# Kernel optimization log

Hardware: AMD Instinct MI355X
Metric: run time of the kernel (lower is better)

The kernel has to match this reference:

```python
import jax, jax.numpy as jnp
import numpy as np

NQ = 4
DIM = 1 << NQ  # 16 statevector amplitudes

def _cnot_perm(c, t):
    idx = np.arange(DIM)
    cbit = (idx >> (NQ - 1 - c)) & 1
    return np.where(cbit == 1, idx ^ (1 << (NQ - 1 - t)), idx)

# BasicEntanglerLayers CNOT ring: (0,1),(1,2),(2,3),(3,0)
CNOT_PERMS = [jnp.asarray(_cnot_perm(q, (q + 1) % NQ)) for q in range(NQ)]
_idx = np.arange(DIM)
SIGNS = jnp.asarray(np.stack([1.0 - 2.0 * ((_idx >> (NQ - 1 - q)) & 1) for q in range(NQ)]).astype(np.float32))  # (NQ, DIM), PauliZ eigenvalues


def _apply_rx(state, theta, q):
    """Apply RX(theta) on wire q. state: (N, DIM) complex64. theta: scalar or (N,)."""
    half = theta * 0.5
    c = jnp.cos(half).astype(jnp.complex64)
    js = (1j * jnp.sin(half)).astype(jnp.complex64)
    if jnp.ndim(theta) == 1:
        c = c[:, None, None]
        js = js[:, None, None]
    d1, d2 = 1 << q, 1 << (NQ - 1 - q)
    st = state.reshape(-1, d1, 2, d2)
    a0, a1 = st[:, :, 0, :], st[:, :, 1, :]
    out = jnp.stack([c * a0 - js * a1, c * a1 - js * a0], axis=2)
    return out.reshape(state.shape)


def circuit(angles, weights):
    """AngleEmbedding(RX) + BasicEntanglerLayers(RX + CNOT ring) + <Z_i>.
    angles: (N, NQ) real. weights: (L, NQ). returns (N, NQ)."""
    N = angles.shape[0]
    state = jnp.zeros((N, DIM), jnp.complex64).at[:, 0].set(1.0)
    for q in range(NQ):  # AngleEmbedding: per-sample RX angles
        state = _apply_rx(state, angles[:, q], q)
    for l in range(weights.shape[0]):  # entangler layers (static count)
        for q in range(NQ):
            state = _apply_rx(state, weights[l, q], q)
        for q in range(NQ):
            state = state[:, CNOT_PERMS[q]]
    probs = jnp.real(state) ** 2 + jnp.imag(state) ** 2
    return probs @ SIGNS.T


def setup_inputs() -> dict:
    key = jax.random.key(0)
    ks = jax.random.split(key, 5)
    B, S = 32, 2048
    TWO_PI = 6.2831853
    return {
        "x": jax.random.normal(ks[0], (B, S, NQ), jnp.float32),
        "weights_Q": jax.random.uniform(ks[1], (1, NQ), jnp.float32) * TWO_PI,
        "weights_K": jax.random.uniform(ks[2], (1, NQ), jnp.float32) * TWO_PI,
        "weights_V": jax.random.uniform(ks[3], (1, NQ), jnp.float32) * TWO_PI,
        "weights_C": jax.random.uniform(ks[4], (1, NQ), jnp.float32) * TWO_PI,
    }


def reference(x, weights_Q, weights_K, weights_V, weights_C):
    B, S, E = x.shape  # E == NQ == 4
    flat = x.reshape(B * S, E)
    Q = circuit(flat, weights_Q).reshape(B, S, E)
    K = circuit(flat, weights_K).reshape(B, S, E)
    V = circuit(flat, weights_V).reshape(B, S, E)
    scores = jnp.einsum('bqe,bke->bqk', Q, K) / (E ** 0.5)
    attn = jax.nn.softmax(scores, axis=-1)
    ctx = jnp.einsum('bqk,bke->bqe', attn, V)
    return circuit(ctx.reshape(B * S, E), weights_C).reshape(B, S, E)
```

## Files before the change

kernel.cpp:

```cpp
#include <hip/hip_runtime.h>

#define DIM 16
#define SEQ 2048
#define CHUNK 256
#define NCHUNK 8
#define RPT 4

typedef float v2f __attribute__((ext_vector_type(2)));

static __device__ __forceinline__ float fexp2(float x) {
#if __has_builtin(__builtin_amdgcn_exp2f)
    return __builtin_amdgcn_exp2f(x);
#else
    return exp2f(x);
#endif
}


template<int P>
__device__ __forceinline__ void rx_bit(float sr[DIM], float si[DIM], float ch, float sh) {
    constexpr int m = 1 << P;
    #pragma unroll
    for (int i = 0; i < DIM; ++i) {
        if ((i & m) == 0) {
            const int j = i | m;
            float r0 = sr[i], i0 = si[i], r1 = sr[j], i1 = si[j];
            sr[i] = fmaf(ch, r0,  sh * i1);
            si[i] = fmaf(ch, i0, -sh * r1);
            sr[j] = fmaf(ch, r1,  sh * i0);
            si[j] = fmaf(ch, i1, -sh * r0);
        }
    }
}

template<int PC, int PT>
__device__ __forceinline__ void cnot_g(float sr[DIM], float si[DIM]) {
    constexpr int cm = 1 << PC, tm = 1 << PT;
    #pragma unroll
    for (int i = 0; i < DIM; ++i) {
        if ((i & cm) && !(i & tm)) {
            const int j = i | tm;
            float t;
            t = sr[i]; sr[i] = sr[j]; sr[j] = t;
            t = si[i]; si[i] = si[j]; si[j] = t;
        }
    }
}

__device__ __forceinline__ void embed(float sr[DIM], float si[DIM], float4 a) {
    #pragma unroll
    for (int i = 0; i < DIM; ++i) { sr[i] = 0.f; si[i] = 0.f; }
    sr[0] = 1.f;
    float ch, sh;
    __sincosf(0.5f * a.x, &sh, &ch); rx_bit<3>(sr, si, ch, sh);
    __sincosf(0.5f * a.y, &sh, &ch); rx_bit<2>(sr, si, ch, sh);
    __sincosf(0.5f * a.z, &sh, &ch); rx_bit<1>(sr, si, ch, sh);
    __sincosf(0.5f * a.w, &sh, &ch); rx_bit<0>(sr, si, ch, sh);
}

__device__ __forceinline__ void layer(float sr[DIM], float si[DIM], float4 w) {
    float ch, sh;
    __sincosf(0.5f * w.x, &sh, &ch); rx_bit<3>(sr, si, ch, sh);
    __sincosf(0.5f * w.y, &sh, &ch); rx_bit<2>(sr, si, ch, sh);
    __sincosf(0.5f * w.z, &sh, &ch); rx_bit<1>(sr, si, ch, sh);
    __sincosf(0.5f * w.w, &sh, &ch); rx_bit<0>(sr, si, ch, sh);
    cnot_g<3,2>(sr, si);
    cnot_g<2,1>(sr, si);
    cnot_g<1,0>(sr, si);
    cnot_g<0,3>(sr, si);
}

__device__ __forceinline__ float4 measure(const float sr[DIM], const float si[DIM]) {
    float e0 = 0.f, e1 = 0.f, e2 = 0.f, e3 = 0.f;
    #pragma unroll
    for (int i = 0; i < DIM; ++i) {
        float p = fmaf(sr[i], sr[i], si[i] * si[i]);
        e0 += (i & 8) ? -p : p;
        e1 += (i & 4) ? -p : p;
        e2 += (i & 2) ? -p : p;
        e3 += (i & 1) ? -p : p;
    }
    return make_float4(e0, e1, e2, e3);
}


__global__ __launch_bounds__(256) void qkv_kernel(
        const float* __restrict__ x,
        const float* __restrict__ wQp, const float* __restrict__ wKp,
        const float* __restrict__ wVp,
        float4* __restrict__ Q, float4* __restrict__ KV) {
    const int i = blockIdx.x * 256 + threadIdx.x;
    const int which = blockIdx.y;
    const float4 xv = ((const float4*)x)[i];
    const float* wp = (which == 0) ? wQp : (which == 1) ? wKp : wVp;
    const float4 w = *(const float4*)wp;

    float sr[DIM], si[DIM];
    embed(sr, si, xv);
    layer(sr, si, w);
    const float4 r = measure(sr, si);

    if (which == 0)      Q[i]          = r;
    else if (which == 1) KV[2 * i]     = r;
    else                 KV[2 * i + 1] = r;
}


__global__ __launch_bounds__(256) void attn_partial(
        const float4* __restrict__ Q, const float4* __restrict__ KV,
        float* __restrict__ pden, float4* __restrict__ pctx, int n) {
    __shared__ float4 kvs[2 * CHUNK];

    const int rg = blockIdx.x;
    const int c  = blockIdx.y;
    const int b  = rg >> 1;

    const float4* src = KV + (size_t)b * (2 * SEQ) + c * (2 * CHUNK);
    for (int t = threadIdx.x; t < 2 * CHUNK; t += 256)
        kvs[t] = src[t];
    __syncthreads();

    const float SC = 0.72134752044f;
    const int row0 = rg * (256 * RPT) + threadIdx.x;

    v2f qa[RPT], qb[RPT];
    #pragma unroll
    for (int j = 0; j < RPT; ++j) {
        const float4 q = Q[row0 + j * 256];
        qa[j] = (v2f){q.x * SC, q.y * SC};
        qb[j] = (v2f){q.z * SC, q.w * SC};
    }

    float den[RPT];
    v2f a01[RPT], a23[RPT];
    #pragma unroll
    for (int j = 0; j < RPT; ++j) {
        den[j] = 0.f;
        a01[j] = (v2f){0.f, 0.f};
        a23[j] = (v2f){0.f, 0.f};
    }

    #pragma unroll 4
    for (int k = 0; k < CHUNK; ++k) {
        const float4 kv = kvs[2 * k];
        const float4 vv = kvs[2 * k + 1];
        const v2f ka = (v2f){kv.x, kv.y}, kb = (v2f){kv.z, kv.w};
        const v2f va = (v2f){vv.x, vv.y}, vb = (v2f){vv.z, vv.w};
        #pragma unroll
        for (int j = 0; j < RPT; ++j) {
            v2f t = __builtin_elementwise_fma(qb[j], kb, qa[j] * ka);
            float e = fexp2(t.x + t.y);
            v2f e2 = (v2f){e, e};
            a01[j] = __builtin_elementwise_fma(e2, va, a01[j]);
            a23[j] = __builtin_elementwise_fma(e2, vb, a23[j]);
            den[j] += e;
        }
    }

    #pragma unroll
    for (int j = 0; j < RPT; ++j) {
        const int row = row0 + j * 256;
        pden[c * n + row] = den[j];
        pctx[c * n + row] = make_float4(a01[j].x, a01[j].y, a23[j].x, a23[j].y);
    }
}


__global__ __launch_bounds__(256) void combine_kernel(
        const float* __restrict__ pden, const float4* __restrict__ pctx,
        const float* __restrict__ wCp, float4* __restrict__ out, int n) {
    const int row = blockIdx.x * 256 + threadIdx.x;

    float d = 0.f;
    float c0 = 0.f, c1 = 0.f, c2 = 0.f, c3 = 0.f;
    #pragma unroll
    for (int c = 0; c < NCHUNK; ++c) {
        d += pden[c * n + row];
        const float4 p = pctx[c * n + row];
        c0 += p.x; c1 += p.y; c2 += p.z; c3 += p.w;
    }
    const float inv = 1.0f / d;
    const float4 ctx = make_float4(c0 * inv, c1 * inv, c2 * inv, c3 * inv);

    const float4 wC = *(const float4*)wCp;
    float sr[DIM], si[DIM];
    embed(sr, si, ctx);
    layer(sr, si, wC);
    out[row] = measure(sr, si);
}


extern "C" void kernel_launch(void* const* d_in, const int* in_sizes, int n_in,
                              void* d_out, int out_size, void* d_ws, size_t ws_size,
                              hipStream_t stream) {
    const float* x  = (const float*)d_in[0];
    const float* wQ = (const float*)d_in[1];
    const float* wK = (const float*)d_in[2];
    const float* wV = (const float*)d_in[3];
    const float* wC = (const float*)d_in[4];

    const int n = in_sizes[0] / 4;
    float4* Q    = (float4*)d_ws;
    float4* KV   = Q + n;
    float4* pctx = KV + 2 * n;
    float*  pden = (float*)(pctx + NCHUNK * n);

    dim3 qgrid(n / 256, 3);
    qkv_kernel<<<qgrid, 256, 0, stream>>>(x, wQ, wK, wV, Q, KV);

    dim3 agrid(n / (256 * RPT), NCHUNK);
    attn_partial<<<agrid, 256, 0, stream>>>(Q, KV, pden, pctx, n);

    combine_kernel<<<n / 256, 256, 0, stream>>>(pden, pctx, wC, (float4*)d_out, n);
}
```

Before: 104.7 us.

## Pair keys in transposed LDS layout, halve rows per thread, closed-form embedding

The attention partial kernel now stores K/V for pairs of keys in a transposed shared-memory layout. Each packed-FMA lane then handles a different key, which removes the horizontal add per score and keeps packed math fully used for the exp-weighted accumulation. Rows per thread drop from 4 to 2, doubling the block count, with an occupancy hint added to launch bounds. The embedding is replaced by a closed-form product state built from sincos products instead of sequential RX gates, cutting ALU work in the QKV and combine kernels.

```diff
diff --git a/kernel.cpp b/kernel.cpp
--- a/kernel.cpp
+++ b/kernel.cpp
@@ -3,10 +3,12 @@
 #define DIM 16
 #define SEQ 2048
 #define CHUNK 256
+#define NPAIR (CHUNK / 2)
 #define NCHUNK 8
-#define RPT 4
+#define RPT 2
 
 typedef float v2f __attribute__((ext_vector_type(2)));
+typedef float v4f __attribute__((ext_vector_type(4)));
 
 static __device__ __forceinline__ float fexp2(float x) {
 #if __has_builtin(__builtin_amdgcn_exp2f)
@@ -48,14 +50,20 @@
 }
 
 __device__ __forceinline__ void embed(float sr[DIM], float si[DIM], float4 a) {
-    #pragma unroll
-    for (int i = 0; i < DIM; ++i) { sr[i] = 0.f; si[i] = 0.f; }
-    sr[0] = 1.f;
-    float ch, sh;
-    __sincosf(0.5f * a.x, &sh, &ch); rx_bit<3>(sr, si, ch, sh);
-    __sincosf(0.5f * a.y, &sh, &ch); rx_bit<2>(sr, si, ch, sh);
-    __sincosf(0.5f * a.z, &sh, &ch); rx_bit<1>(sr, si, ch, sh);
-    __sincosf(0.5f * a.w, &sh, &ch); rx_bit<0>(sr, si, ch, sh);
+    float c0, s0, c1, s1, c2, s2, c3, s3;
+    __sincosf(0.5f * a.x, &s0, &c0);
+    __sincosf(0.5f * a.y, &s1, &c1);
+    __sincosf(0.5f * a.z, &s2, &c2);
+    __sincosf(0.5f * a.w, &s3, &c3);
+    float A[4] = {c0 * c1, c0 * s1, s0 * c1, s0 * s1};
+    float B[4] = {c2 * c3, c2 * s3, s2 * c3, s2 * s3};
+    #pragma unroll
+    for (int idx = 0; idx < DIM; ++idx) {
+        const float p = A[idx >> 2] * B[idx & 3];
+        const int m = __builtin_popcount(idx) & 3;
+        sr[idx] = (m == 0) ? p : (m == 2) ? -p : 0.f;
+        si[idx] = (m == 1) ? -p : (m == 3) ? p : 0.f;
+    }
 }
 
 __device__ __forceinline__ void layer(float sr[DIM], float si[DIM], float4 w) {
@@ -106,62 +114,78 @@
 }
 
 
-__global__ __launch_bounds__(256) void attn_partial(
+__global__ __launch_bounds__(256, 4) void attn_partial(
         const float4* __restrict__ Q, const float4* __restrict__ KV,
         float* __restrict__ pden, float4* __restrict__ pctx, int n) {
-    __shared__ float4 kvs[2 * CHUNK];
+    __shared__ float4 kvs[4 * NPAIR];
 
     const int rg = blockIdx.x;
     const int c  = blockIdx.y;
-    const int b  = rg >> 1;
-
-    const float4* src = KV + (size_t)b * (2 * SEQ) + c * (2 * CHUNK);
-    for (int t = threadIdx.x; t < 2 * CHUNK; t += 256)
-        kvs[t] = src[t];
+    const int b  = rg >> 2;
+
+    const float4* KVc = KV + (size_t)b * (2 * SEQ) + c * (2 * CHUNK);
+    if (threadIdx.x < NPAIR) {
+        const int p = threadIdx.x;
+        const float4 K0 = KVc[4 * p + 0];
+        const float4 V0 = KVc[4 * p + 1];
+        const float4 K1 = KVc[4 * p + 2];
+        const float4 V1 = KVc[4 * p + 3];
+        kvs[4 * p + 0] = make_float4(K0.x, K1.x, K0.y, K1.y);
+        kvs[4 * p + 1] = make_float4(K0.z, K1.z, K0.w, K1.w);
+        kvs[4 * p + 2] = make_float4(V0.x, V1.x, V0.y, V1.y);
+        kvs[4 * p + 3] = make_float4(V0.z, V1.z, V0.w, V1.w);
+    }
     __syncthreads();
 
     const float SC = 0.72134752044f;
     const int row0 = rg * (256 * RPT) + threadIdx.x;
 
-    v2f qa[RPT], qb[RPT];
+    v2f qx[RPT], qy[RPT], qz[RPT], qw[RPT];
     #pragma unroll
     for (int j = 0; j < RPT; ++j) {
         const float4 q = Q[row0 + j * 256];
-        qa[j] = (v2f){q.x * SC, q.y * SC};
-        qb[j] = (v2f){q.z * SC, q.w * SC};
-    }
-
-    float den[RPT];
-    v2f a01[RPT], a23[RPT];
+        qx[j] = (v2f){q.x * SC, q.x * SC};
+        qy[j] = (v2f){q.y * SC, q.y * SC};
+        qz[j] = (v2f){q.z * SC, q.z * SC};
+        qw[j] = (v2f){q.w * SC, q.w * SC};
+    }
+
+    v2f den[RPT], ax[RPT], ay[RPT], az[RPT], aw[RPT];
     #pragma unroll
     for (int j = 0; j < RPT; ++j) {
-        den[j] = 0.f;
-        a01[j] = (v2f){0.f, 0.f};
-        a23[j] = (v2f){0.f, 0.f};
-    }
-
+        den[j] = (v2f){0.f, 0.f};
+        ax[j] = den[j]; ay[j] = den[j]; az[j] = den[j]; aw[j] = den[j];
+    }
+
+    const v4f* kvp = (const v4f*)kvs;
     #pragma unroll 4
-    for (int k = 0; k < CHUNK; ++k) {
-        const float4 kv = kvs[2 * k];
-        const float4 vv = kvs[2 * k + 1];
-        const v2f ka = (v2f){kv.x, kv.y}, kb = (v2f){kv.z, kv.w};
-        const v2f va = (v2f){vv.x, vv.y}, vb = (v2f){vv.z, vv.w};
+    for (int p = 0; p < NPAIR; ++p) {
+        const v4f kA = kvp[4 * p + 0];
+        const v4f kB = kvp[4 * p + 1];
+        const v4f vA = kvp[4 * p + 2];
+        const v4f vB = kvp[4 * p + 3];
+        const v2f kx = kA.xy, ky = kA.zw, kz = kB.xy, kw = kB.zw;
+        const v2f vx = vA.xy, vy = vA.zw, vz = vB.xy, vw = vB.zw;
         #pragma unroll
         for (int j = 0; j < RPT; ++j) {
-            v2f t = __builtin_elementwise_fma(qb[j], kb, qa[j] * ka);
-            float e = fexp2(t.x + t.y);
-            v2f e2 = (v2f){e, e};
-            a01[j] = __builtin_elementwise_fma(e2, va, a01[j]);
-            a23[j] = __builtin_elementwise_fma(e2, vb, a23[j]);
+            v2f s = __builtin_elementwise_fma(qy[j], ky, qx[j] * kx);
+            s     = __builtin_elementwise_fma(qz[j], kz, s);
+            s     = __builtin_elementwise_fma(qw[j], kw, s);
+            const v2f e = (v2f){fexp2(s.x), fexp2(s.y)};
             den[j] += e;
+            ax[j] = __builtin_elementwise_fma(e, vx, ax[j]);
+            ay[j] = __builtin_elementwise_fma(e, vy, ay[j]);
+            az[j] = __builtin_elementwise_fma(e, vz, az[j]);
+            aw[j] = __builtin_elementwise_fma(e, vw, aw[j]);
         }
     }
 
     #pragma unroll
     for (int j = 0; j < RPT; ++j) {
         const int row = row0 + j * 256;
-        pden[c * n + row] = den[j];
-        pctx[c * n + row] = make_float4(a01[j].x, a01[j].y, a23[j].x, a23[j].y);
+        pden[c * n + row] = den[j].x + den[j].y;
+        pctx[c * n + row] = make_float4(ax[j].x + ax[j].y, ay[j].x + ay[j].y,
+                                        az[j].x + az[j].y, aw[j].x + aw[j].y);
     }
 }
 
```

After: 101.8 us. 1.03x faster.
